# Kernel optimization log

Measured on AMD Instinct MI355X. Metric: run time of the kernel, lower is better.

## Reference

```python
import jax, jax.numpy as jnp
import numpy as np

N = 32768          # total nodes
C = 384            # in/out channels == embed_dim
E = 384            # embed_dim
G = 12             # tetrahedral group size
H = 1              # effective_num_heads = num_heads // G
D = 32             # head_dim = (E // G) // H
P = D // 2         # RoPE rotation pairs
SD = 3             # spatial dims
NUM_GRAPHS = 64
AVG_NUM_NODES = float(N) / NUM_GRAPHS  # 512.0, passed as avg_num_nodes


def rope_apply(t, phase):
    # t: [N,G,H,D], phase: [N,G,H,P]; rotate consecutive (even,odd) pairs
    c, s = jnp.cos(phase), jnp.sin(phase)
    t2 = t.reshape(*t.shape[:-1], P, 2)
    x1, x2 = t2[..., 0], t2[..., 1]
    rot = jnp.stack([x1 * c - x2 * s, x1 * s + x2 * c], axis=-1)
    return rot.reshape(t.shape)


def setup_inputs() -> dict:
    key = jax.random.key(0)
    ks = jax.random.split(key, 8)
    x = jax.random.normal(ks[0], (N, C), jnp.float32)
    pos = jax.random.normal(ks[1], (N, SD), jnp.float32)
    batch = jnp.sort(jax.random.randint(ks[2], (N,), 0, NUM_GRAPHS)).astype(jnp.int32)
    sc = 1.0 / np.sqrt(C).astype(np.float32)
    Wq = jax.random.normal(ks[3], (C, E), jnp.float32) * sc
    Wv = jax.random.normal(ks[4], (C, E), jnp.float32) * sc
    Wo = jax.random.normal(ks[5], (E, C), jnp.float32) * (1.0 / np.sqrt(E).astype(np.float32))
    freqs = jax.random.normal(ks[6], (G, H, P, SD), jnp.float32)  # freq_sigma = 1.0
    return {
        'x': x, 'pos': pos, 'batch': batch,
        'Wq': Wq, 'bq': jnp.zeros((E,), jnp.float32),
        'Wv': Wv, 'bv': jnp.zeros((E,), jnp.float32),
        'Wo': Wo, 'bo': jnp.zeros((C,), jnp.float32),
        'freqs': freqs,
    }


def reference(x, pos, batch, Wq, bq, Wv, bv, Wo, bo, freqs):
    # projections -> [N, G, H, D]
    q = (x @ Wq + bq).reshape(N, G, H, D)
    v = (x @ Wv + bv).reshape(N, G, H, D)
    # RoPE phase from positions: [N, G, H, P]
    phase = jnp.einsum('ns,ghps->nghp', pos, freqs)
    q = rope_apply(q, phase)
    k = rope_apply(jnp.ones_like(q), phase)  # use_key=False -> k_raw = ones
    # linear attention: per-node outer product, then per-graph segment sum
    kv = jnp.einsum('nghd,nghe->nghde', k, v)              # [N,G,H,D,D]
    kv_kernel = jax.ops.segment_sum(kv, batch, num_segments=NUM_GRAPHS)
    kv_kernel = kv_kernel / AVG_NUM_NODES                  # mean_aggregation=False
    out = jnp.einsum('nghd,nghde->nghe', q, kv_kernel[batch])
    out = out.reshape(N, -1)
    return out @ Wo + bo
```

## Files before the change

### kernel.cpp

```cpp
#include <hip/hip_runtime.h>


#define N_NODES 32768
#define K_DIM   384
#define P_PAIR  16
#define NUM_GRAPHS 64

typedef unsigned short u16;
typedef __bf16 bf16x8 __attribute__((ext_vector_type(8)));
typedef float  f32x4  __attribute__((ext_vector_type(4)));
typedef float  f32x16 __attribute__((ext_vector_type(16)));
typedef __attribute__((address_space(3))) void       lds_void;
typedef const __attribute__((address_space(1))) void gbl_void;

__device__ __forceinline__ u16 f2bf(float f) {
    unsigned int i = __float_as_uint(f);
    unsigned int r = i + 0x7FFFu + ((i >> 16) & 1u);
    return (u16)(r >> 16);
}
__device__ __forceinline__ float bf2f(u16 u) {
    union { unsigned int i; float f; } x;
    x.i = ((unsigned int)u) << 16;
    return x.f;
}

__global__ void prep(const float* __restrict__ x,
                     const float* __restrict__ Wq, const float* __restrict__ Wv,
                     const float* __restrict__ Wo,
                     u16* __restrict__ xb, u16* __restrict__ WqvT,
                     u16* __restrict__ WoT) {
    int b = blockIdx.x;
    if (b < 6144) {
        int i = (b * 256 + threadIdx.x) * 8;
        float4 a0 = *reinterpret_cast<const float4*>(x + i);
        float4 a1 = *reinterpret_cast<const float4*>(x + i + 4);
        union { u16 u[8]; float4 v; } pk;
        pk.u[0] = f2bf(a0.x); pk.u[1] = f2bf(a0.y);
        pk.u[2] = f2bf(a0.z); pk.u[3] = f2bf(a0.w);
        pk.u[4] = f2bf(a1.x); pk.u[5] = f2bf(a1.y);
        pk.u[6] = f2bf(a1.z); pk.u[7] = f2bf(a1.w);
        *reinterpret_cast<float4*>(xb + i) = pk.v;
        return;
    }
    __shared__ float ld[32][33];
    const int tb  = b - 6144;
    const int mat = tb / 144;
    const int tl  = tb % 144;
    const int tr  = tl / 12, tc = tl % 12;
    const float* src = (mat == 0) ? Wq : (mat == 1) ? Wv : Wo;
    u16* dst = (mat == 2) ? WoT : WqvT;
    const int n_off = (mat == 1) ? 384 : 0;

    const int t = threadIdx.x;
    const int c = t & 31, r = t >> 5;
#pragma unroll
    for (int i = 0; i < 4; i++) {
        int r0 = r + (i << 3);
        ld[r0][c] = src[(tr * 32 + r0) * 384 + tc * 32 + c];
    }
    __syncthreads();
    const int ck = t & 31;
#pragma unroll
    for (int i = 0; i < 4; i++) {
        int cn = r + (i << 3);
        dst[(size_t)(n_off + tc * 32 + cn) * 384 + tr * 32 + ck] = f2bf(ld[ck][cn]);
    }
}

#define GEMM_CORE(A_PTR, B_PTR)                                                  \
    __shared__ __align__(1024) u16 T[16384];                                     \
    const int tid = threadIdx.x;                                                 \
    const int w = tid >> 6, lane = tid & 63;                                     \
    const int wr = (w >> 1) << 6, wc = (w & 1) << 6;                             \
    const int lm = lane & 15, q = lane >> 4;                                     \
    const int srow = lane >> 2, sc8 = (lane & 3) << 3;                           \
    f32x4 acc[4][4];                                                             \
    _Pragma("unroll") for (int i = 0; i < 4; i++)                                \
    _Pragma("unroll") for (int j = 0; j < 4; j++)                                \
    _Pragma("unroll") for (int r = 0; r < 4; r++) acc[i][j][r] = 0.0f;           \
    for (int k0 = 0; k0 < K_DIM; k0 += 64) {                                     \
        __syncthreads();                                                         \
        _Pragma("unroll")                                                        \
        for (int s = w; s < 32; s += 4) {                                        \
            int row  = ((s & 7) << 4) + srow;                                    \
            int half = (s >> 3) & 1;                                             \
            const u16* gp = ((s >> 4) ? (B_PTR) + (size_t)(n0 + row) * K_DIM     \
                                      : (A_PTR) + (size_t)(m0 + row) * K_DIM)    \
                            + k0 + (half << 5) + sc8;                            \
            __builtin_amdgcn_global_load_lds((gbl_void*)gp,                      \
                                             (lds_void*)&T[s << 9], 16, 0, 0);   \
        }                                                                        \
        __syncthreads();                                                         \
        _Pragma("unroll")                                                        \
        for (int h = 0; h < 2; h++) {                                            \
            bf16x8 af[4], bfr[4];                                                \
            _Pragma("unroll") for (int i = 0; i < 4; i++) {                      \
                af[i]  = *reinterpret_cast<const bf16x8*>(                       \
                    &T[(h << 12) + (wr + i * 16 + lm) * 32 + q * 8]);            \
                bfr[i] = *reinterpret_cast<const bf16x8*>(                       \
                    &T[8192 + (h << 12) + (wc + i * 16 + lm) * 32 + q * 8]);     \
            }                                                                    \
            _Pragma("unroll") for (int i = 0; i < 4; i++)                        \
            _Pragma("unroll") for (int j = 0; j < 4; j++)                        \
                acc[i][j] = __builtin_amdgcn_mfma_f32_16x16x32_bf16(             \
                    af[i], bfr[j], acc[i][j], 0, 0, 0);                          \
        }                                                                        \
    }

__global__ __launch_bounds__(256) void gemm_qv(
    const u16* __restrict__ A, const u16* __restrict__ Bt,
    const float* __restrict__ bq, const float* __restrict__ bv,
    u16* __restrict__ Qw, u16* __restrict__ Vd) {
    const int b = blockIdx.x;
    const int xcd = b & 7, jj = b >> 3;
    const int by = xcd * 32 + jj / 6, bx = jj % 6;
    const int m0 = by << 7, n0 = bx << 7;
    GEMM_CORE(A, Bt)
    u16* Cq = (n0 < 384) ? Qw : Vd;
    const float* bias = (n0 < 384) ? bq : bv;
    const int coff = (n0 < 384) ? 0 : 384;
#pragma unroll
    for (int j = 0; j < 4; j++) {
        int gc = n0 + wc + j * 16 + lm - coff;
        float bs = bias[gc];
#pragma unroll
        for (int i = 0; i < 4; i++) {
            int gr = m0 + wr + i * 16 + q * 4;
#pragma unroll
            for (int r = 0; r < 4; r++)
                Cq[(size_t)(gr + r) * 384 + gc] = f2bf(acc[i][j][r] + bs);
        }
    }
}

__global__ __launch_bounds__(256) void gemm_out(
    const u16* __restrict__ A, const u16* __restrict__ Bt,
    const float* __restrict__ bias, float* __restrict__ Cmat) {
    const int b = blockIdx.x;
    const int xcd = b & 7, jj = b >> 3;
    const int by = xcd * 32 + jj / 3, bx = jj % 3;
    const int m0 = by << 7, n0 = bx << 7;
    GEMM_CORE(A, Bt)
#pragma unroll
    for (int j = 0; j < 4; j++) {
        int gc = n0 + wc + j * 16 + lm;
        float bs = bias[gc];
#pragma unroll
        for (int i = 0; i < 4; i++) {
            int gr = m0 + wr + i * 16 + q * 4;
#pragma unroll
            for (int r = 0; r < 4; r++)
                Cmat[(size_t)(gr + r) * 384 + gc] = acc[i][j][r] + bs;
        }
    }
}

__global__ __launch_bounds__(256) void kv_mfma(
    const u16* __restrict__ V, const float* __restrict__ pos,
    const int* __restrict__ batch, const float* __restrict__ freqs,
    float* __restrict__ KV) {
    const int bid = blockIdx.x;
    const int xcd = bid & 7, jj = bid >> 3;
    const int g = (xcd << 3) + jj / 12, grp = jj % 12;

    const int tid = threadIdx.x;
    const int w = tid >> 6, lane = tid & 63;
    const int hi = lane >> 5, de = lane & 31;
    const int p = de >> 1, sgn = de & 1;

    const float f0 = freqs[(grp * P_PAIR + p) * 3 + 0];
    const float f1 = freqs[(grp * P_PAIR + p) * 3 + 1];
    const float f2 = freqs[(grp * P_PAIR + p) * 3 + 2];

    int s0 = 0, s1 = N_NODES;
    while (s0 < s1) { int m = (s0 + s1) >> 1; if (batch[m] < g) s0 = m + 1; else s1 = m; }
    const int start = s0;
    int e0 = start, e1 = N_NODES;
    while (e0 < e1) { int m = (e0 + e1) >> 1; if (batch[m] < g + 1) e0 = m + 1; else e1 = m; }
    const int end = e0;

    __shared__ __align__(1024) u16 vbuf[2048];
    __shared__ float posb[192];
    __shared__ __align__(16) float red[4096];

    f32x16 acc;
#pragma unroll
    for (int r = 0; r < 16; r++) acc[r] = 0.0f;

    const int nl0 = w * 16 + hi * 8;

    for (int c = start; c < end; c += 64) {
        __syncthreads();
        if (tid < 192) {
            int i = c * 3 + tid;
            posb[tid] = (i < 3 * N_NODES) ? pos[i] : 0.0f;
        }
        {
            int r = tid >> 2;
            int nn = c + r;
            const u16* gp = V + (size_t)nn * K_DIM + (grp << 5) + ((tid & 3) << 3);
            if (nn < N_NODES)
                __builtin_amdgcn_global_load_lds((gbl_void*)gp,
                                                 (lds_void*)&vbuf[w << 9], 16, 0, 0);
        }
        __syncthreads();

        union { bf16x8 v; u16 u[8]; } A, B;
#pragma unroll
        for (int j = 0; j < 8; j++) {
            int nl = nl0 + j;
            int n = c + nl;
            float ph = posb[nl * 3 + 0] * f0 + posb[nl * 3 + 1] * f1
                     + posb[nl * 3 + 2] * f2;
            float sn, cs;
            __sincosf(ph, &sn, &cs);
            float kd = sgn ? (sn + cs) : (cs - sn);
            bool valid = n < end;
            A.u[j] = valid ? f2bf(kd) : (u16)0;
            B.u[j] = valid ? vbuf[(nl << 5) + de] : (u16)0;
        }
        acc = __builtin_amdgcn_mfma_f32_32x32x16_bf16(A.v, B.v, acc, 0, 0, 0);
    }

#pragma unroll
    for (int r = 0; r < 16; r++) {
        int d = (r & 3) + ((r >> 2) << 3) + (hi << 2);
        red[(w << 10) + (d << 5) + de] = acc[r];
    }
    __syncthreads();
    {
        int i4 = tid << 2;
        f32x4 a0 = *reinterpret_cast<const f32x4*>(&red[i4]);
        f32x4 a1 = *reinterpret_cast<const f32x4*>(&red[1024 + i4]);
        f32x4 a2 = *reinterpret_cast<const f32x4*>(&red[2048 + i4]);
        f32x4 a3 = *reinterpret_cast<const f32x4*>(&red[3072 + i4]);
        f32x4 s = (a0 + a1 + a2 + a3) * (1.0f / 512.0f);
        *reinterpret_cast<f32x4*>(&KV[((size_t)(g * 12 + grp) << 10) + i4]) = s;
    }
}

__global__ __launch_bounds__(256) void attn_mfma(
    u16* __restrict__ Qw, const float* __restrict__ pos,
    const int* __restrict__ batch, const float* __restrict__ freqs,
    const float* __restrict__ KV) {
    const int bid = blockIdx.x;
    const int xcd = bid & 7, jj = bid >> 3;
    const int chunk = (xcd << 5) + jj / 12, grp = jj % 12;
    const int nbase = chunk << 7;

    const int tid = threadIdx.x;
    const int w = tid >> 6, lane = tid & 63;
    const int hi = lane >> 5, de = lane & 31;

    __shared__ float sfreq[48];
    __shared__ __align__(16) float red[4096];

    if (tid < 48) sfreq[tid] = freqs[grp * 48 + tid];

    const int node = nbase + (w << 5) + de;
    const float p0 = pos[node * 3 + 0];
    const float p1 = pos[node * 3 + 1];
    const float p2 = pos[node * 3 + 2];
    const int bnode = batch[node];
    const int g0 = batch[nbase + (w << 5)];
    const int g1 = batch[nbase + (w << 5) + 31];

    union { bf16x8 v; u16 u[8]; } qlo, qhi, alo, ahi;
    {
        const u16* qp = Qw + (size_t)node * K_DIM + (grp << 5) + (hi << 3);
        qlo.v = *reinterpret_cast<const bf16x8*>(qp);
        qhi.v = *reinterpret_cast<const bf16x8*>(qp + 16);
    }
    __syncthreads();
#pragma unroll
    for (int z = 0; z < 4; z++) {
        const int pl = (hi << 2) + z;
        const float* F  = &sfreq[pl * 3];
        const float* F2 = &sfreq[(8 + pl) * 3];
        float sn, cs, sn2, cs2;
        __sincosf(p0 * F[0]  + p1 * F[1]  + p2 * F[2],  &sn,  &cs);
        __sincosf(p0 * F2[0] + p1 * F2[1] + p2 * F2[2], &sn2, &cs2);
        float x1 = bf2f(qlo.u[2 * z]), x2 = bf2f(qlo.u[2 * z + 1]);
        alo.u[2 * z]     = f2bf(x1 * cs - x2 * sn);
        alo.u[2 * z + 1] = f2bf(x1 * sn + x2 * cs);
        float y1 = bf2f(qhi.u[2 * z]), y2 = bf2f(qhi.u[2 * z + 1]);
        ahi.u[2 * z]     = f2bf(y1 * cs2 - y2 * sn2);
        ahi.u[2 * z + 1] = f2bf(y1 * sn2 + y2 * cs2);
    }

    f32x16 oacc;
#pragma unroll
    for (int r = 0; r < 16; r++) oacc[r] = 0.0f;
    for (int g = g0; g <= g1; g++) {
        const bool msk = (bnode == g);
        union { bf16x8 v; u16 u[8]; } ml, mh, bl, bh;
#pragma unroll
        for (int j = 0; j < 8; j++) {
            ml.u[j] = msk ? alo.u[j] : (u16)0;
            mh.u[j] = msk ? ahi.u[j] : (u16)0;
        }
        const float* kvp = KV + (((size_t)(g * 12 + grp)) << 10) + de;
#pragma unroll
        for (int j = 0; j < 8; j++) {
            bl.u[j] = f2bf(kvp[(hi * 8 + j) << 5]);
            bh.u[j] = f2bf(kvp[(16 + hi * 8 + j) << 5]);
        }
        oacc = __builtin_amdgcn_mfma_f32_32x32x16_bf16(ml.v, bl.v, oacc, 0, 0, 0);
        oacc = __builtin_amdgcn_mfma_f32_32x32x16_bf16(mh.v, bh.v, oacc, 0, 0, 0);
    }

#pragma unroll
    for (int r = 0; r < 16; r++) {
        int rl = (r & 3) + ((r >> 2) << 3) + (hi << 2);
        red[((w << 5) + rl) * 32 + de] = oacc[r];
    }
    __syncthreads();
    {
        const int row = tid >> 1, half = tid & 1;
        union { u16 u[16]; float4 v[2]; } pk;
#pragma unroll
        for (int z = 0; z < 16; z++)
            pk.u[z] = f2bf(red[row * 32 + half * 16 + z]);
        float4* dst = reinterpret_cast<float4*>(
            Qw + (size_t)(nbase + row) * K_DIM + (grp << 5) + (half << 4));
        dst[0] = pk.v[0];
        dst[1] = pk.v[1];
    }
}

extern "C" void kernel_launch(void* const* d_in, const int* in_sizes, int n_in,
                              void* d_out, int out_size, void* d_ws, size_t ws_size,
                              hipStream_t stream) {
    const float* x     = (const float*)d_in[0];
    const float* pos   = (const float*)d_in[1];
    const int*   batch = (const int*)d_in[2];
    const float* Wq    = (const float*)d_in[3];
    const float* bq    = (const float*)d_in[4];
    const float* Wv    = (const float*)d_in[5];
    const float* bv    = (const float*)d_in[6];
    const float* Wo    = (const float*)d_in[7];
    const float* bo    = (const float*)d_in[8];
    const float* fr    = (const float*)d_in[9];
    float* out = (float*)d_out;

    char* ws = (char*)d_ws;
    float* KV   = (float*)(ws);
    u16*   WqvT = (u16*)(ws + 3145728);
    u16*   WoT  = (u16*)(ws + 3735552);
    u16*   Qw   = (u16*)(ws + 4030464);
    u16*   Vd   = (u16*)d_out;
    u16*   xb   = (u16*)d_out + N_NODES * 384;

    prep<<<dim3(6576), dim3(256), 0, stream>>>(x, Wq, Wv, Wo, xb, WqvT, WoT);
    gemm_qv<<<dim3(1536), dim3(256), 0, stream>>>(xb, WqvT, bq, bv, Qw, Vd);
    kv_mfma<<<dim3(768), dim3(256), 0, stream>>>(Vd, pos, batch, fr, KV);
    attn_mfma<<<dim3(3072), dim3(256), 0, stream>>>(Qw, pos, batch, fr, KV);
    gemm_out<<<dim3(768), dim3(256), 0, stream>>>(Qw, WoT, bo, out);
}
```

Before: 195.2 us.

## Fuse fp32-to-bf16 conversion of x into the QV projection GEMM

Removes the separate pass that converts x from fp32 to bf16. The QV GEMM now loads fp32 tiles of x straight into LDS and converts them to bf16 in registers with v_cvt_pk_bf16_f32 before the MFMAs. This saves writing and re-reading a bf16 copy of x (about 25 MB of traffic). In exchange, each x tile is read from global memory six times as fp32 (once per N block), which doubles the A-side bytes. It also puts conversion work and larger LDS reads in the inner loop.

```diff
diff --git a/kernel.cpp b/kernel.cpp
--- a/kernel.cpp
+++ b/kernel.cpp
@@ -24,26 +24,11 @@
     return x.f;
 }
 
-__global__ void prep(const float* __restrict__ x,
-                     const float* __restrict__ Wq, const float* __restrict__ Wv,
+__global__ void prep(const float* __restrict__ Wq, const float* __restrict__ Wv,
                      const float* __restrict__ Wo,
-                     u16* __restrict__ xb, u16* __restrict__ WqvT,
-                     u16* __restrict__ WoT) {
-    int b = blockIdx.x;
-    if (b < 6144) {
-        int i = (b * 256 + threadIdx.x) * 8;
-        float4 a0 = *reinterpret_cast<const float4*>(x + i);
-        float4 a1 = *reinterpret_cast<const float4*>(x + i + 4);
-        union { u16 u[8]; float4 v; } pk;
-        pk.u[0] = f2bf(a0.x); pk.u[1] = f2bf(a0.y);
-        pk.u[2] = f2bf(a0.z); pk.u[3] = f2bf(a0.w);
-        pk.u[4] = f2bf(a1.x); pk.u[5] = f2bf(a1.y);
-        pk.u[6] = f2bf(a1.z); pk.u[7] = f2bf(a1.w);
-        *reinterpret_cast<float4*>(xb + i) = pk.v;
-        return;
-    }
+                     u16* __restrict__ WqvT, u16* __restrict__ WoT) {
     __shared__ float ld[32][33];
-    const int tb  = b - 6144;
+    const int tb  = blockIdx.x;
     const int mat = tb / 144;
     const int tl  = tb % 144;
     const int tr  = tl / 12, tc = tl % 12;
@@ -108,14 +93,73 @@
     }
 
 __global__ __launch_bounds__(256) void gemm_qv(
-    const u16* __restrict__ A, const u16* __restrict__ Bt,
+    const float* __restrict__ X, const u16* __restrict__ Bt,
     const float* __restrict__ bq, const float* __restrict__ bv,
     u16* __restrict__ Qw, u16* __restrict__ Vd) {
     const int b = blockIdx.x;
     const int xcd = b & 7, jj = b >> 3;
     const int by = xcd * 32 + jj / 6, bx = jj % 6;
     const int m0 = by << 7, n0 = bx << 7;
-    GEMM_CORE(A, Bt)
+
+    __shared__ __align__(1024) u16 T[24576];
+    float* Af = reinterpret_cast<float*>(T);
+    const int tid = threadIdx.x;
+    const int w = tid >> 6, lane = tid & 63;
+    const int wr = (w >> 1) << 6, wc = (w & 1) << 6;
+    const int lm = lane & 15, q = lane >> 4;
+    const int srow = lane >> 2, sc8 = (lane & 3) << 3;
+    const int arow = lane >> 4, ac4 = (lane & 15) << 2;
+
+    f32x4 acc[4][4];
+#pragma unroll
+    for (int i = 0; i < 4; i++)
+#pragma unroll
+    for (int j = 0; j < 4; j++)
+#pragma unroll
+    for (int r = 0; r < 4; r++) acc[i][j][r] = 0.0f;
+
+    for (int k0 = 0; k0 < K_DIM; k0 += 64) {
+        __syncthreads();
+#pragma unroll
+        for (int s = w; s < 32; s += 4) {
+            const float* gp = X + (size_t)(m0 + (s << 2) + arow) * K_DIM + k0 + ac4;
+            __builtin_amdgcn_global_load_lds((gbl_void*)gp,
+                                             (lds_void*)&Af[s << 8], 16, 0, 0);
+        }
+#pragma unroll
+        for (int s = w; s < 16; s += 4) {
+            int row  = ((s & 7) << 4) + srow;
+            int half = (s >> 3) & 1;
+            const u16* gp = Bt + (size_t)(n0 + row) * K_DIM + k0 + (half << 5) + sc8;
+            __builtin_amdgcn_global_load_lds((gbl_void*)gp,
+                                             (lds_void*)&T[16384 + (s << 9)], 16, 0, 0);
+        }
+        __syncthreads();
+#pragma unroll
+        for (int h = 0; h < 2; h++) {
+            bf16x8 af[4], bfr[4];
+#pragma unroll
+            for (int i = 0; i < 4; i++) {
+                const float* ap = &Af[(wr + i * 16 + lm) * 64 + (h << 5) + q * 8];
+                f32x4 a0 = *reinterpret_cast<const f32x4*>(ap);
+                f32x4 a1 = *reinterpret_cast<const f32x4*>(ap + 4);
+                union { bf16x8 v; unsigned int u[4]; } pk;
+                asm("v_cvt_pk_bf16_f32 %0, %1, %2" : "=v"(pk.u[0]) : "v"(a0[0]), "v"(a0[1]));
+                asm("v_cvt_pk_bf16_f32 %0, %1, %2" : "=v"(pk.u[1]) : "v"(a0[2]), "v"(a0[3]));
+                asm("v_cvt_pk_bf16_f32 %0, %1, %2" : "=v"(pk.u[2]) : "v"(a1[0]), "v"(a1[1]));
+                asm("v_cvt_pk_bf16_f32 %0, %1, %2" : "=v"(pk.u[3]) : "v"(a1[2]), "v"(a1[3]));
+                af[i] = pk.v;
+                bfr[i] = *reinterpret_cast<const bf16x8*>(
+                    &T[16384 + (h << 12) + (wc + i * 16 + lm) * 32 + q * 8]);
+            }
+#pragma unroll
+            for (int i = 0; i < 4; i++)
+#pragma unroll
+            for (int j = 0; j < 4; j++)
+                acc[i][j] = __builtin_amdgcn_mfma_f32_16x16x32_bf16(
+                    af[i], bfr[j], acc[i][j], 0, 0, 0);
+        }
+    }
     u16* Cq = (n0 < 384) ? Qw : Vd;
     const float* bias = (n0 < 384) ? bq : bv;
     const int coff = (n0 < 384) ? 0 : 384;
@@ -349,10 +393,9 @@
     u16*   WoT  = (u16*)(ws + 3735552);
     u16*   Qw   = (u16*)(ws + 4030464);
     u16*   Vd   = (u16*)d_out;
-    u16*   xb   = (u16*)d_out + N_NODES * 384;
-
-    prep<<<dim3(6576), dim3(256), 0, stream>>>(x, Wq, Wv, Wo, xb, WqvT, WoT);
-    gemm_qv<<<dim3(1536), dim3(256), 0, stream>>>(xb, WqvT, bq, bv, Qw, Vd);
+
+    prep<<<dim3(432), dim3(256), 0, stream>>>(Wq, Wv, Wo, WqvT, WoT);
+    gemm_qv<<<dim3(1536), dim3(256), 0, stream>>>(x, WqvT, bq, bv, Qw, Vd);
     kv_mfma<<<dim3(768), dim3(256), 0, stream>>>(Vd, pos, batch, fr, KV);
     attn_mfma<<<dim3(3072), dim3(256), 0, stream>>>(Qw, pos, batch, fr, KV);
     gemm_out<<<dim3(768), dim3(256), 0, stream>>>(Qw, WoT, bo, out);
```

New measurement: 212.6 us. +8.9%, slower.
